# Optimization experiments

Measured on AMD Instinct MI355X. Metric: run time of the kernel, lower is better.

The kernel has to match this reference:

```python
import jax, jax.numpy as jnp
import numpy as np

B, L, D = 2, 2048, 2048
H, Hd = 16, 128


def _rotary_cos_sin(max_len, dim, base=10000.0):
    inv_freq = 1.0 / (base ** (np.arange(0, dim, 2, dtype=np.float32) / dim))
    t = np.arange(max_len, dtype=np.float32)
    freqs = np.outer(t, inv_freq)                      # [L, dim/2]
    emb = np.concatenate([freqs, freqs], axis=-1)      # [L, dim]
    cos = np.cos(emb)[None, None]                      # [1,1,L,dim]
    sin = np.sin(emb)[None, None]
    return jnp.asarray(cos), jnp.asarray(sin)


def setup_inputs() -> dict:
    key = jax.random.key(0)
    ks = jax.random.split(key, 5)
    hidden_states = jax.random.normal(ks[0], (B, L, D), dtype=jnp.float32)
    cos, sin = _rotary_cos_sin(L, Hd)
    s = 1.0 / np.sqrt(D)
    wq = jax.random.normal(ks[1], (H * Hd, D), dtype=jnp.float32) * s
    wk = jax.random.normal(ks[2], (H * Hd, D), dtype=jnp.float32) * s
    wv = jax.random.normal(ks[3], (H * Hd, D), dtype=jnp.float32) * s
    wo = jax.random.normal(ks[4], (D, H * Hd), dtype=jnp.float32) * s
    return {"hidden_states": hidden_states, "cos": cos, "sin": sin,
            "wq": wq, "wk": wk, "wv": wv, "wo": wo}


def _rotate_half(x):
    x1, x2 = jnp.split(x, 2, axis=-1)
    return jnp.concatenate([-x2, x1], axis=-1)


def reference(hidden_states, cos, sin, wq, wk, wv, wo):
    b, l, d = hidden_states.shape
    # QKV projections -> [B, H, L, Hd]
    q = (hidden_states @ wq.T).reshape(b, l, H, Hd).transpose(0, 2, 1, 3)
    k = (hidden_states @ wk.T).reshape(b, l, H, Hd).transpose(0, 2, 1, 3)
    v = (hidden_states @ wv.T).reshape(b, l, H, Hd).transpose(0, 2, 1, 3)
    c = cos[:, :, :l, :]
    s = sin[:, :, :l, :]
    q = q * c + _rotate_half(q) * s
    k = k * c + _rotate_half(k) * s
    # SDPA (non-causal, default scale = 1/sqrt(head_dim))
    scale = 1.0 / jnp.sqrt(jnp.asarray(Hd, dtype=q.dtype))
    scores = jnp.einsum('bhqd,bhkd->bhqk', q, k) * scale
    attn = jax.nn.softmax(scores, axis=-1)
    out = jnp.einsum('bhqk,bhkd->bhqd', attn, v)       # [B,H,L,Hd]
    out = out.transpose(0, 2, 1, 3).reshape(b, l, H * Hd)
    return out @ wo.T
```

## Files before the change

### kernel.cpp

```cpp
#include <hip/hip_runtime.h>

constexpr int Bb = 2;
constexpr int Ll = 2048;
constexpr int Dd = 2048;
constexpr int Hh = 16;
constexpr int Hd = 128;
constexpr int M  = Bb * Ll;

typedef __attribute__((ext_vector_type(8)))  short s16x8;
typedef __attribute__((ext_vector_type(4)))  float f32x4;
typedef __attribute__((ext_vector_type(16))) float f32x16;

__device__ __forceinline__ unsigned short f2bf(float f) {
    union { float f; unsigned u; } v; v.f = f;
    unsigned r = v.u + 0x7fffu + ((v.u >> 16) & 1u);
    return (unsigned short)(r >> 16);
}
__device__ __forceinline__ float bf2f(unsigned short b) {
    union { unsigned u; float f; } v; v.u = ((unsigned)b) << 16;
    return v.f;
}
__device__ __forceinline__ float fast_exp2(float x) {
#if __has_builtin(__builtin_amdgcn_exp2f)
    return __builtin_amdgcn_exp2f(x);
#else
    return exp2f(x);
#endif
}

__device__ __forceinline__ void gld16(const void* g, void* l) {
#if __has_builtin(__builtin_amdgcn_global_load_lds)
    __builtin_amdgcn_global_load_lds(
        (const __attribute__((address_space(1))) unsigned int*)g,
        (__attribute__((address_space(3))) unsigned int*)l, 16, 0, 0);
#else
    int lane = threadIdx.x & 63;
    ((int4*)l)[lane] = ((const int4*)g)[0];
#endif
}

__global__ __launch_bounds__(256)
void f2bf_kernel(const float* __restrict__ in, unsigned short* __restrict__ out, int n)
{
    int i = (blockIdx.x * 256 + threadIdx.x) * 4;
    if (i < n) {
        float4 v = *(const float4*)(in + i);
        ushort4 o;
        o.x = f2bf(v.x); o.y = f2bf(v.y); o.z = f2bf(v.z); o.w = f2bf(v.w);
        *(ushort4*)(out + i) = o;
    }
}

template<int MODE>
__global__ __launch_bounds__(512, 2)
void mfma_gemm(const unsigned short* __restrict__ A,
               const unsigned short* __restrict__ W0,
               const unsigned short* __restrict__ W1,
               const unsigned short* __restrict__ W2,
               unsigned short* __restrict__ O0,
               unsigned short* __restrict__ O1,
               unsigned short* __restrict__ O2,
               float* __restrict__ FO)
{
    constexpr int K  = 2048;
    constexpr int NT = K / 64;
    constexpr int SLOT_US = 24576;

    const unsigned short* W = W0;
    if (MODE == 0)
        W = (blockIdx.z == 0) ? W0 : (blockIdx.z == 1) ? W1 : W2;

    __shared__ unsigned short lds[3 * SLOT_US];

    const int t    = threadIdx.x;
    const int w    = t >> 6, lane = t & 63;
    const int wm   = w >> 1, wn = w & 1;
    const int m0   = blockIdx.y * 256, n0 = blockIdx.x * 128;
    const int r16  = lane & 15, q4 = lane >> 4;
    const int lxor = (r16 & 7) << 4;

    const int srow8 = lane >> 3;
    const int sgcol = (((lane & 7) ^ srow8) << 4);
    const char* Agb = (const char*)A;
    const char* Wgb = (const char*)W;

    f32x4 acc[4][4];
#pragma unroll
    for (int i = 0; i < 4; ++i)
#pragma unroll
        for (int j = 0; j < 4; ++j)
            acc[i][j] = (f32x4){0.f, 0.f, 0.f, 0.f};

    s16x8 af[4], bf[4];

#define STAGE_A(tt, sl, p) do {                                              \
    int ia_ = w * 4 + (p);                                                   \
    gld16(Agb + (size_t)(m0 + ia_ * 8 + srow8) * (K * 2) + (tt) * 128 + sgcol, \
          &lds[(sl) * SLOT_US + ia_ * 512]); } while (0)
#define STAGE_B(tt, sl, p) do {                                              \
    int ib_ = w * 2 + (p);                                                   \
    gld16(Wgb + (size_t)(n0 + ib_ * 8 + srow8) * (K * 2) + (tt) * 128 + sgcol, \
          &lds[(sl) * SLOT_US + 16384 + ib_ * 512]); } while (0)

#define LOAD_FRAGS(sl, ksub) do {                                            \
    const char* Ab_ = (const char*)&lds[(sl) * SLOT_US];                     \
    const char* Bb_ = (const char*)&lds[(sl) * SLOT_US + 16384];             \
    int cc_ = ((ksub) * 64 + q4 * 16) ^ lxor;                                \
    _Pragma("unroll") for (int mi = 0; mi < 4; ++mi)                         \
        af[mi] = *(const s16x8*)(Ab_ + (wm * 64 + mi * 16 + r16) * 128 + cc_); \
    _Pragma("unroll") for (int ni = 0; ni < 4; ++ni)                         \
        bf[ni] = *(const s16x8*)(Bb_ + (wn * 64 + ni * 16 + r16) * 128 + cc_); \
} while (0)

#define DO_MFMA() do {                                                       \
    __builtin_amdgcn_s_setprio(1);                                           \
    _Pragma("unroll") for (int mi = 0; mi < 4; ++mi)                         \
    _Pragma("unroll") for (int ni = 0; ni < 4; ++ni)                         \
        acc[mi][ni] = __builtin_amdgcn_mfma_f32_16x16x32_bf16(                \
            af[mi], bf[ni], acc[mi][ni], 0, 0, 0);                           \
    __builtin_amdgcn_s_setprio(0);                                           \
} while (0)

    STAGE_A(0, 0, 0); STAGE_A(0, 0, 1); STAGE_B(0, 0, 0);
    STAGE_A(0, 0, 2); STAGE_A(0, 0, 3); STAGE_B(0, 0, 1);
    STAGE_A(1, 1, 0); STAGE_A(1, 1, 1); STAGE_B(1, 1, 0);
    STAGE_A(1, 1, 2); STAGE_A(1, 1, 3); STAGE_B(1, 1, 1);
    asm volatile("s_waitcnt vmcnt(6)" ::: "memory");
    __builtin_amdgcn_s_barrier();
    asm volatile("" ::: "memory");

    int slot = 0;
    for (int tt = 0; tt < NT; ++tt) {
        int snx = slot + 2; if (snx >= 3) snx -= 3;
        const bool pf = (tt + 2 < NT);

        LOAD_FRAGS(slot, 0);
        if (pf) { STAGE_A(tt + 2, snx, 0); STAGE_A(tt + 2, snx, 1); STAGE_B(tt + 2, snx, 0); }
        asm volatile("" ::: "memory");
        __builtin_amdgcn_s_barrier();
        asm volatile("s_waitcnt lgkmcnt(0)" ::: "memory");
        DO_MFMA();
        asm volatile("" ::: "memory");
        __builtin_amdgcn_s_barrier();
        asm volatile("" ::: "memory");

        LOAD_FRAGS(slot, 1);
        if (pf) { STAGE_A(tt + 2, snx, 2); STAGE_A(tt + 2, snx, 3); STAGE_B(tt + 2, snx, 1); }
        asm volatile("" ::: "memory");
        __builtin_amdgcn_s_barrier();
        asm volatile("s_waitcnt lgkmcnt(0)" ::: "memory");
        DO_MFMA();
        if (pf)               asm volatile("s_waitcnt vmcnt(6)" ::: "memory");
        else if (tt + 1 < NT) asm volatile("s_waitcnt vmcnt(0)" ::: "memory");
        asm volatile("" ::: "memory");
        __builtin_amdgcn_s_barrier();
        asm volatile("" ::: "memory");

        slot = (slot == 2) ? 0 : slot + 1;
    }

#undef STAGE_A
#undef STAGE_B
#undef LOAD_FRAGS
#undef DO_MFMA

    const int wrow = wm * 64, wcol = wn * 64;
    if (MODE == 0) {
        if (blockIdx.z < 2) {
            unsigned short* O = (blockIdx.z == 0) ? O0 : O1;
#pragma unroll
            for (int mi = 0; mi < 4; ++mi)
#pragma unroll
                for (int ni = 0; ni < 4; ++ni) {
                    int n = n0 + wcol + ni * 16 + r16;
                    int h = n >> 7, d = n & 127;
#pragma unroll
                    for (int r = 0; r < 4; ++r) {
                        int m = m0 + wrow + mi * 16 + q4 * 4 + r;
                        int b = m >> 11, l = m & 2047;
                        O[(((size_t)b * Hh + h) * Ll + l) * Hd + d] =
                            f2bf(acc[mi][ni][r]);
                    }
                }
        } else {
#pragma unroll
            for (int mi = 0; mi < 4; ++mi) {
                int mb = m0 + wrow + mi * 16 + q4 * 4;
                int b = mb >> 11, l = mb & 2047;
#pragma unroll
                for (int ni = 0; ni < 4; ++ni) {
                    int n = n0 + wcol + ni * 16 + r16;
                    int h = n >> 7, d = n & 127;
                    ushort4 pk;
                    pk.x = f2bf(acc[mi][ni][0]);
                    pk.y = f2bf(acc[mi][ni][1]);
                    pk.z = f2bf(acc[mi][ni][2]);
                    pk.w = f2bf(acc[mi][ni][3]);
                    *(ushort4*)&O2[(((size_t)b * Hh + h) * Hd + d) * Ll + l] = pk;
                }
            }
        }
    } else {
#pragma unroll
        for (int mi = 0; mi < 4; ++mi)
#pragma unroll
            for (int ni = 0; ni < 4; ++ni) {
                int n = n0 + wcol + ni * 16 + r16;
#pragma unroll
                for (int r = 0; r < 4; ++r) {
                    int m = m0 + wrow + mi * 16 + q4 * 4 + r;
                    FO[(size_t)m * Dd + n] = acc[mi][ni][r];
                }
            }
    }
}

__global__ __launch_bounds__(256)
void rope_bf16(unsigned short* __restrict__ q, unsigned short* __restrict__ k,
               const float* __restrict__ cosb, const float* __restrict__ sinb)
{
    const float QS = 0.1275175f;
    const int t = threadIdx.x;
    int rblk = blockIdx.x;
    unsigned short* base;
    float sc;
    if (rblk < 4096) { base = q; sc = QS; }
    else             { base = k; sc = 1.0f; rblk -= 4096; }

    const int row = rblk * 16 + (t >> 4);
    const int l   = row & (Ll - 1);
    const int d0  = (t & 15) * 8;
    unsigned short* xr = base + (size_t)row * Hd;

    s16x8 v0 = *(const s16x8*)(xr + d0);
    s16x8 vp = *(const s16x8*)(xr + (d0 ^ 64));
    const float* cp = cosb + (size_t)l * Hd + d0;
    const float* sp = sinb + (size_t)l * Hd + d0;
    float4 c0 = *(const float4*)cp,       c1 = *(const float4*)(cp + 4);
    float4 sa = *(const float4*)sp,       sb = *(const float4*)(sp + 4);
    const float cc[8] = {c0.x, c0.y, c0.z, c0.w, c1.x, c1.y, c1.z, c1.w};
    const float ss[8] = {sa.x, sa.y, sa.z, sa.w, sb.x, sb.y, sb.z, sb.w};
    const float sgn = (d0 < 64) ? -1.f : 1.f;

    s16x8 o;
#pragma unroll
    for (int j = 0; j < 8; ++j) {
        float a = bf2f((unsigned short)v0[j]);
        float p = bf2f((unsigned short)vp[j]);
        float res = fmaf(a, cc[j], sgn * p * ss[j]) * sc;
        o[j] = (short)f2bf(res);
    }
    asm volatile("" ::: "memory");
    *(s16x8*)(xr + d0) = o;
}

__global__ __launch_bounds__(256)
void flash_attn(const unsigned short* __restrict__ q,
                const unsigned short* __restrict__ k,
                const unsigned short* __restrict__ vT,
                unsigned short* __restrict__ ctx)
{
    __shared__ unsigned short Ks[2][64 * 128];
    __shared__ unsigned short Vs[2][128 * 64];
    __shared__ unsigned short Ps[4][32 * 64];

    const int t = threadIdx.x;
    const int w = t >> 6, lane = t & 63;
    const int n32 = lane & 31, half = lane >> 5;
    const int bh = blockIdx.x >> 4;
    const int l0 = (blockIdx.x & 15) * 128;

    const unsigned short* qb = q  + ((size_t)bh * Ll + l0 + w * 32) * Hd;
    const unsigned short* kb = k  + (size_t)bh * Ll * Hd;
    const unsigned short* vb = vT + (size_t)bh * Hd * Ll;

    const int k_r = lane >> 4, k_u = lane & 15;
    const int v_r = lane >> 3, v_u = lane & 7;

#define STAGE(J0, bsel) do {                                                  \
    _Pragma("unroll") for (int p = 0; p < 4; ++p) {                           \
        int j_ = w * 4 + p;                                                   \
        int row_ = j_ * 4 + k_r;                                              \
        gld16(kb + (size_t)((J0) + row_) * Hd + ((k_u ^ (row_ & 7)) * 8),     \
              &Ks[bsel][j_ * 512]);                                           \
    }                                                                         \
    _Pragma("unroll") for (int p = 0; p < 4; ++p) {                           \
        int j_ = w * 4 + p;                                                   \
        int row_ = j_ * 8 + v_r;                                              \
        gld16(vb + (size_t)row_ * Ll + (J0) + ((v_u ^ (row_ & 7)) * 8),       \
              &Vs[bsel][j_ * 512]);                                           \
    }                                                                         \
} while (0)

    s16x8 qf[8];
#pragma unroll
    for (int ks = 0; ks < 8; ++ks)
        qf[ks] = *(const s16x8*)(qb + (size_t)n32 * Hd + ks * 16 + half * 8);

    f32x16 o[4];
    float lacc[16];
#pragma unroll
    for (int nt = 0; nt < 4; ++nt)
#pragma unroll
        for (int r = 0; r < 16; ++r) o[nt][r] = 0.f;
#pragma unroll
    for (int r = 0; r < 16; ++r) lacc[r] = 0.f;

    unsigned short* Pw = Ps[w];
    const int psw = (n32 & 7) << 3;

    STAGE(0, 0);
    __syncthreads();

    int buf = 0;
    for (int j0 = 0; j0 < Ll; j0 += 64) {
        if (j0 + 64 < Ll) STAGE(j0 + 64, buf ^ 1);

        f32x16 s0, s1;
#pragma unroll
        for (int r = 0; r < 16; ++r) { s0[r] = 0.f; s1[r] = 0.f; }
        __builtin_amdgcn_s_setprio(1);
#pragma unroll
        for (int ks = 0; ks < 8; ++ks) {
            int kc = (ks * 16 + half * 8) ^ psw;
            s16x8 b0 = *(const s16x8*)&Ks[buf][n32 * 128 + kc];
            s16x8 b1 = *(const s16x8*)&Ks[buf][(32 + n32) * 128 + kc];
            s0 = __builtin_amdgcn_mfma_f32_32x32x16_bf16(qf[ks], b0, s0, 0, 0, 0);
            s1 = __builtin_amdgcn_mfma_f32_32x32x16_bf16(qf[ks], b1, s1, 0, 0, 0);
        }
        __builtin_amdgcn_s_setprio(0);

#pragma unroll
        for (int r = 0; r < 16; ++r) {
            int mrow = (r & 3) + 8 * (r >> 2) + 4 * half;
            int sw = (mrow & 7) << 3;
            float p0 = fast_exp2(s0[r]);
            float p1 = fast_exp2(s1[r]);
            lacc[r] += p0 + p1;
            union { float f; unsigned u; } u0, u1;
            u0.f = p0; u1.f = p1;
            Pw[mrow * 64 + (n32 ^ sw)]        = (unsigned short)((u0.u + 0x8000u) >> 16);
            Pw[mrow * 64 + ((32 + n32) ^ sw)] = (unsigned short)((u1.u + 0x8000u) >> 16);
        }

        __builtin_amdgcn_s_setprio(1);
#pragma unroll
        for (int kst = 0; kst < 4; ++kst) {
            int cc = (kst * 16 + half * 8) ^ psw;
            s16x8 pf2 = *(const s16x8*)&Pw[n32 * 64 + cc];
#pragma unroll
            for (int nt = 0; nt < 4; ++nt) {
                s16x8 vf = *(const s16x8*)&Vs[buf][(nt * 32 + n32) * 64 + cc];
                o[nt] = __builtin_amdgcn_mfma_f32_32x32x16_bf16(pf2, vf, o[nt], 0, 0, 0);
            }
        }
        __builtin_amdgcn_s_setprio(0);

        __syncthreads();
        buf ^= 1;
    }

#undef STAGE

    float linv[16];
#pragma unroll
    for (int r = 0; r < 16; ++r) {
        float s = lacc[r];
        s += __shfl_xor(s, 1, 64);
        s += __shfl_xor(s, 2, 64);
        s += __shfl_xor(s, 4, 64);
        s += __shfl_xor(s, 8, 64);
        s += __shfl_xor(s, 16, 64);
        linv[r] = 1.0f / s;
    }

    const int b = bh >> 4, h = bh & 15;
#pragma unroll
    for (int nt = 0; nt < 4; ++nt)
#pragma unroll
        for (int r = 0; r < 16; ++r) {
            int mrow = (r & 3) + 8 * (r >> 2) + 4 * half;
            int lq = l0 + w * 32 + mrow;
            ctx[((size_t)(b * Ll + lq)) * Dd + h * Hd + nt * 32 + n32] =
                f2bf(o[nt][r] * linv[r]);
        }
}

extern "C" void kernel_launch(void* const* d_in, const int* in_sizes, int n_in,
                              void* d_out, int out_size, void* d_ws, size_t ws_size,
                              hipStream_t stream)
{
    const float* hs   = (const float*)d_in[0];
    const float* cosb = (const float*)d_in[1];
    const float* sinb = (const float*)d_in[2];
    const float* wq   = (const float*)d_in[3];
    const float* wk   = (const float*)d_in[4];
    const float* wv   = (const float*)d_in[5];
    const float* wo   = (const float*)d_in[6];
    float* out = (float*)d_out;

    char* ws = (char*)d_ws;
    unsigned short* Xb  = (unsigned short*)(ws);
    unsigned short* Wqb = (unsigned short*)(ws + (16ull << 20));
    unsigned short* Wkb = (unsigned short*)(ws + (24ull << 20));
    unsigned short* Wvb = (unsigned short*)(ws + (32ull << 20));
    unsigned short* Wob = (unsigned short*)(ws + (40ull << 20));
    unsigned short* qb  = (unsigned short*)(ws + (48ull << 20));
    unsigned short* kb  = (unsigned short*)(ws + (64ull << 20));
    unsigned short* vTb = (unsigned short*)(ws + (80ull << 20));
    unsigned short* ctx = Xb;

    const int nX = M * Dd;
    const int nW = Dd * Dd;

    f2bf_kernel<<<dim3(nX / 4 / 256), dim3(256), 0, stream>>>(hs, Xb, nX);
    f2bf_kernel<<<dim3(nW / 4 / 256), dim3(256), 0, stream>>>(wq, Wqb, nW);
    f2bf_kernel<<<dim3(nW / 4 / 256), dim3(256), 0, stream>>>(wk, Wkb, nW);
    f2bf_kernel<<<dim3(nW / 4 / 256), dim3(256), 0, stream>>>(wv, Wvb, nW);
    f2bf_kernel<<<dim3(nW / 4 / 256), dim3(256), 0, stream>>>(wo, Wob, nW);

    mfma_gemm<0><<<dim3(Dd / 128, M / 256, 3), dim3(512), 0, stream>>>(
        Xb, Wqb, Wkb, Wvb, qb, kb, vTb, nullptr);

    rope_bf16<<<dim3(2 * (Bb * Hh * Ll) / 16), dim3(256), 0, stream>>>(
        qb, kb, cosb, sinb);

    flash_attn<<<dim3(Bb * Hh * (Ll / 128)), dim3(256), 0, stream>>>(qb, kb, vTb, ctx);

    mfma_gemm<1><<<dim3(Dd / 128, M / 256, 1), dim3(512), 0, stream>>>(
        ctx, Wob, nullptr, nullptr, nullptr, nullptr, nullptr, out);
}
```

Baseline: 402.3 us.

## Fuse QKV projections into one wide GEMM with 256x192 tiles

Treats the contiguous Wq/Wk/Wv bf16 buffers as one 6144x2048 weight matrix. A dedicated QKV kernel uses 256x192 block tiles, with each of 8 waves computing a 128x48 sub-tile. It replaces the previous triple-buffered pipeline with a simpler double-buffered one and routes outputs to Q, K or transposed V by column range. The larger tile aims to raise operand reuse and cut the block count. In exchange it uses about 112KB of LDS per block, which likely limits occupancy to one block per CU, and its pipelining is less aggressive. The output projection becomes a separate non-templated kernel with the same logic as before.

```diff
diff --git a/kernel.cpp b/kernel.cpp
--- a/kernel.cpp
+++ b/kernel.cpp
@@ -51,24 +51,151 @@
     }
 }
 
-template<int MODE>
 __global__ __launch_bounds__(512, 2)
-void mfma_gemm(const unsigned short* __restrict__ A,
-               const unsigned short* __restrict__ W0,
-               const unsigned short* __restrict__ W1,
-               const unsigned short* __restrict__ W2,
-               unsigned short* __restrict__ O0,
-               unsigned short* __restrict__ O1,
-               unsigned short* __restrict__ O2,
-               float* __restrict__ FO)
+void mfma_gemm_qkv(const unsigned short* __restrict__ A,
+                   const unsigned short* __restrict__ Wall,
+                   unsigned short* __restrict__ Oq,
+                   unsigned short* __restrict__ Ok,
+                   unsigned short* __restrict__ Ov)
+{
+    constexpr int K  = 2048;
+    constexpr int NT = K / 64;
+    constexpr int BM = 256, BN = 192;
+    constexpr int SLOT_US = (BM + BN) * 64;
+
+    __shared__ unsigned short lds[2 * SLOT_US];
+
+    const int t    = threadIdx.x;
+    const int w    = t >> 6, lane = t & 63;
+    const int wm   = w >> 2, wn = w & 3;
+    const int m0   = blockIdx.y * BM, n0 = blockIdx.x * BN;
+    const int r16  = lane & 15, q4 = lane >> 4;
+    const int lxor = (r16 & 7) << 4;
+
+    const int srow8 = lane >> 3;
+    const int sgcol = (((lane & 7) ^ srow8) << 4);
+    const char* Agb = (const char*)A;
+    const char* Wgb = (const char*)Wall;
+
+    f32x4 acc[8][3];
+#pragma unroll
+    for (int i = 0; i < 8; ++i)
+#pragma unroll
+        for (int j = 0; j < 3; ++j)
+            acc[i][j] = (f32x4){0.f, 0.f, 0.f, 0.f};
+
+#define STAGE(tt, sl) do {                                                   \
+    _Pragma("unroll") for (int p = 0; p < 4; ++p) {                          \
+        int ia_ = w * 4 + p;                                                 \
+        gld16(Agb + (size_t)(m0 + ia_ * 8 + srow8) * (K * 2) + (tt) * 128 + sgcol, \
+              &lds[(sl) * SLOT_US + ia_ * 512]);                             \
+    }                                                                        \
+    _Pragma("unroll") for (int p = 0; p < 3; ++p) {                          \
+        int ib_ = w * 3 + p;                                                 \
+        gld16(Wgb + (size_t)(n0 + ib_ * 8 + srow8) * (K * 2) + (tt) * 128 + sgcol, \
+              &lds[(sl) * SLOT_US + BM * 64 + ib_ * 512]);                   \
+    }                                                                        \
+} while (0)
+
+    STAGE(0, 0);
+    asm volatile("s_waitcnt vmcnt(0)" ::: "memory");
+    __builtin_amdgcn_s_barrier();
+    asm volatile("" ::: "memory");
+
+    int slot = 0;
+    for (int tt = 0; tt < NT; ++tt) {
+        const char* Ab = (const char*)&lds[slot * SLOT_US];
+        const char* Bp = (const char*)&lds[slot * SLOT_US + BM * 64];
+        const int c0 = (q4 * 16) ^ lxor;
+        const int c1 = (64 + q4 * 16) ^ lxor;
+
+        s16x8 a0[8], a1[8], b0[3], b1[3];
+#pragma unroll
+        for (int mi = 0; mi < 8; ++mi) {
+            int rb = (wm * 128 + mi * 16 + r16) * 128;
+            a0[mi] = *(const s16x8*)(Ab + rb + c0);
+        }
+#pragma unroll
+        for (int ni = 0; ni < 3; ++ni) {
+            int rb = (wn * 48 + ni * 16 + r16) * 128;
+            b0[ni] = *(const s16x8*)(Bp + rb + c0);
+        }
+        if (tt + 1 < NT) STAGE(tt + 1, slot ^ 1);
+#pragma unroll
+        for (int mi = 0; mi < 8; ++mi) {
+            int rb = (wm * 128 + mi * 16 + r16) * 128;
+            a1[mi] = *(const s16x8*)(Ab + rb + c1);
+        }
+#pragma unroll
+        for (int ni = 0; ni < 3; ++ni) {
+            int rb = (wn * 48 + ni * 16 + r16) * 128;
+            b1[ni] = *(const s16x8*)(Bp + rb + c1);
+        }
+
+        __builtin_amdgcn_s_setprio(1);
+#pragma unroll
+        for (int mi = 0; mi < 8; ++mi)
+#pragma unroll
+            for (int ni = 0; ni < 3; ++ni)
+                acc[mi][ni] = __builtin_amdgcn_mfma_f32_16x16x32_bf16(
+                    a0[mi], b0[ni], acc[mi][ni], 0, 0, 0);
+#pragma unroll
+        for (int mi = 0; mi < 8; ++mi)
+#pragma unroll
+            for (int ni = 0; ni < 3; ++ni)
+                acc[mi][ni] = __builtin_amdgcn_mfma_f32_16x16x32_bf16(
+                    a1[mi], b1[ni], acc[mi][ni], 0, 0, 0);
+        __builtin_amdgcn_s_setprio(0);
+
+        asm volatile("s_waitcnt vmcnt(0)" ::: "memory");
+        __builtin_amdgcn_s_barrier();
+        asm volatile("" ::: "memory");
+        slot ^= 1;
+    }
+#undef STAGE
+
+#pragma unroll
+    for (int ni = 0; ni < 3; ++ni) {
+        int nb   = n0 + wn * 48 + ni * 16;
+        int nsel = nb >> 11;
+        int nr   = nb & 2047;
+        int h    = nr >> 7;
+        int d    = (nr & 127) + r16;
+        if (nsel < 2) {
+            unsigned short* O = nsel ? Ok : Oq;
+#pragma unroll
+            for (int mi = 0; mi < 8; ++mi)
+#pragma unroll
+                for (int r = 0; r < 4; ++r) {
+                    int m = m0 + wm * 128 + mi * 16 + q4 * 4 + r;
+                    int b = m >> 11, l = m & 2047;
+                    O[(((size_t)b * Hh + h) * Ll + l) * Hd + d] =
+                        f2bf(acc[mi][ni][r]);
+                }
+        } else {
+#pragma unroll
+            for (int mi = 0; mi < 8; ++mi) {
+                int mb = m0 + wm * 128 + mi * 16 + q4 * 4;
+                int b = mb >> 11, l = mb & 2047;
+                ushort4 pk;
+                pk.x = f2bf(acc[mi][ni][0]);
+                pk.y = f2bf(acc[mi][ni][1]);
+                pk.z = f2bf(acc[mi][ni][2]);
+                pk.w = f2bf(acc[mi][ni][3]);
+                *(ushort4*)&Ov[(((size_t)b * Hh + h) * Hd + d) * Ll + l] = pk;
+            }
+        }
+    }
+}
+
+__global__ __launch_bounds__(512, 2)
+void mfma_gemm_out(const unsigned short* __restrict__ A,
+                   const unsigned short* __restrict__ W,
+                   float* __restrict__ FO)
 {
     constexpr int K  = 2048;
     constexpr int NT = K / 64;
     constexpr int SLOT_US = 24576;
-
-    const unsigned short* W = W0;
-    if (MODE == 0)
-        W = (blockIdx.z == 0) ? W0 : (blockIdx.z == 1) ? W1 : W2;
 
     __shared__ unsigned short lds[3 * SLOT_US];
 
@@ -158,61 +285,22 @@
 
         slot = (slot == 2) ? 0 : slot + 1;
     }
-
 #undef STAGE_A
 #undef STAGE_B
 #undef LOAD_FRAGS
 #undef DO_MFMA
 
-    const int wrow = wm * 64, wcol = wn * 64;
-    if (MODE == 0) {
-        if (blockIdx.z < 2) {
-            unsigned short* O = (blockIdx.z == 0) ? O0 : O1;
-#pragma unroll
-            for (int mi = 0; mi < 4; ++mi)
-#pragma unroll
-                for (int ni = 0; ni < 4; ++ni) {
-                    int n = n0 + wcol + ni * 16 + r16;
-                    int h = n >> 7, d = n & 127;
-#pragma unroll
-                    for (int r = 0; r < 4; ++r) {
-                        int m = m0 + wrow + mi * 16 + q4 * 4 + r;
-                        int b = m >> 11, l = m & 2047;
-                        O[(((size_t)b * Hh + h) * Ll + l) * Hd + d] =
-                            f2bf(acc[mi][ni][r]);
-                    }
-                }
-        } else {
-#pragma unroll
-            for (int mi = 0; mi < 4; ++mi) {
-                int mb = m0 + wrow + mi * 16 + q4 * 4;
-                int b = mb >> 11, l = mb & 2047;
-#pragma unroll
-                for (int ni = 0; ni < 4; ++ni) {
-                    int n = n0 + wcol + ni * 16 + r16;
-                    int h = n >> 7, d = n & 127;
-                    ushort4 pk;
-                    pk.x = f2bf(acc[mi][ni][0]);
-                    pk.y = f2bf(acc[mi][ni][1]);
-                    pk.z = f2bf(acc[mi][ni][2]);
-                    pk.w = f2bf(acc[mi][ni][3]);
-                    *(ushort4*)&O2[(((size_t)b * Hh + h) * Hd + d) * Ll + l] = pk;
-                }
+#pragma unroll
+    for (int mi = 0; mi < 4; ++mi)
+#pragma unroll
+        for (int ni = 0; ni < 4; ++ni) {
+            int n = n0 + wn * 64 + ni * 16 + r16;
+#pragma unroll
+            for (int r = 0; r < 4; ++r) {
+                int m = m0 + wm * 64 + mi * 16 + q4 * 4 + r;
+                FO[(size_t)m * Dd + n] = acc[mi][ni][r];
             }
         }
-    } else {
-#pragma unroll
-        for (int mi = 0; mi < 4; ++mi)
-#pragma unroll
-            for (int ni = 0; ni < 4; ++ni) {
-                int n = n0 + wcol + ni * 16 + r16;
-#pragma unroll
-                for (int r = 0; r < 4; ++r) {
-                    int m = m0 + wrow + mi * 16 + q4 * 4 + r;
-                    FO[(size_t)m * Dd + n] = acc[mi][ni][r];
-                }
-            }
-    }
 }
 
 __global__ __launch_bounds__(256)
@@ -359,7 +447,6 @@
         __syncthreads();
         buf ^= 1;
     }
-
 #undef STAGE
 
     float linv[16];
@@ -419,14 +506,14 @@
     f2bf_kernel<<<dim3(nW / 4 / 256), dim3(256), 0, stream>>>(wv, Wvb, nW);
     f2bf_kernel<<<dim3(nW / 4 / 256), dim3(256), 0, stream>>>(wo, Wob, nW);
 
-    mfma_gemm<0><<<dim3(Dd / 128, M / 256, 3), dim3(512), 0, stream>>>(
-        Xb, Wqb, Wkb, Wvb, qb, kb, vTb, nullptr);
+    mfma_gemm_qkv<<<dim3(6144 / 192, M / 256), dim3(512), 0, stream>>>(
+        Xb, Wqb, qb, kb, vTb);
 
     rope_bf16<<<dim3(2 * (Bb * Hh * Ll) / 16), dim3(256), 0, stream>>>(
         qb, kb, cosb, sinb);
 
     flash_attn<<<dim3(Bb * Hh * (Ll / 128)), dim3(256), 0, stream>>>(qb, kb, vTb, ctx);
 
-    mfma_gemm<1><<<dim3(Dd / 128, M / 256, 1), dim3(512), 0, stream>>>(
-        ctx, Wob, nullptr, nullptr, nullptr, nullptr, nullptr, out);
-}
+    mfma_gemm_out<<<dim3(Dd / 128, M / 256), dim3(512), 0, stream>>>(
+        ctx, Wob, out);
+}
```

Result: faster. 391.9 us (-2.6%).
